# Optimization experiments

Measured on AMD Instinct MI355X. Metric: run time of the kernel, lower is better.

The kernel has to match this reference:

```python
import jax, jax.numpy as jnp
import numpy as np

B, L, N, C = 32, 12, 2048, 3
D = 64          # embed_dim
TOPK = 8
NK = 16         # n_kernel
TOD = 288
DOW = 7
OUT = 12        # output_len
NLAYER = 3
HS = 3 * D + TOPK * D + D        # spatial_hidden_dim = 768
HT = 4 * D + TOPK * D + D        # temporal_hidden_dim = 832
HC = int(100 * 0.1 * np.log(N / 0.1))  # EmbeddingTrainer bottleneck = 99
EPS = 1e-8


def setup_inputs() -> dict:
    key = jax.random.key(0)
    ks = jax.random.split(key, 20)
    r = lambda i, shape, s=0.02: jax.random.normal(ks[i], shape, jnp.float32) * s
    return dict(
        history_data=jax.random.uniform(ks[0], (B, L, N, C), jnp.float32),
        future_data=jax.random.uniform(ks[1], (B, OUT, N, C), jnp.float32),
        node_emb=r(2, (N, D), 0.1),
        et_w1=r(3, (HC, N)), et_b1=jnp.zeros((HC,), jnp.float32),
        et_w2=r(4, (N, HC)), et_b2=jnp.zeros((N,), jnp.float32),
        tod_emb=r(5, (TOD, D), 0.1), dow_emb=r(6, (DOW, D), 0.1),
        ts_w=r(7, (D, L), 0.1),
        feature_emb=r(8, (NK, D), 0.1),
        kernels=r(9, (NK, L), 0.1),
        sp_w=r(10, (D, HS)), sp_b=jnp.zeros((D,), jnp.float32),
        mlp_w1=r(11, (NLAYER, HT, HT), 0.01), mlp_b1=jnp.zeros((NLAYER, HT), jnp.float32),
        mlp_w2=r(12, (NLAYER, HT, HT), 0.01), mlp_b2=jnp.zeros((NLAYER, HT), jnp.float32),
        treg_w=r(13, (OUT, L), 0.1), treg_b=jnp.zeros((OUT,), jnp.float32),
        sreg_w=r(14, (OUT, HT), 0.02), sreg_b=jnp.zeros((OUT,), jnp.float32),
        daily_data=r(15, (TOD, N), 0.01), weekly_data=r(16, (DOW, N), 0.01),
        w_spatial=jnp.full((N,), 0.5, jnp.float32),
        batch_seen=0, epoch=0, train=1,
    )


def _forward(history_data, future_data, node_emb, et_w1, et_b1, et_w2, et_b2,
             tod_emb, dow_emb, ts_w, feature_emb, kernels, sp_w, sp_b,
             mlp_w1, mlp_b1, mlp_w2, mlp_b2, treg_w, treg_b, sreg_w, sreg_b,
             daily_data, weekly_data, w_spatial):
    x_in = history_data[..., 0]                              # (B,L,N)
    # --- temporal embeddings at last step ---
    tod_idx = (history_data[:, -1, :, 1] * TOD).astype(jnp.int32)   # (B,N)
    dow_idx = (history_data[:, -1, :, 2] * DOW).astype(jnp.int32)
    tid = tod_emb[tod_idx]                                   # (B,N,D)
    diw = dow_emb[dow_idx]
    # --- time-series embedding (1x1 conv over L channels) ---
    ts_emb = jnp.einsum('bln,dl->bdn', x_in, ts_w)           # (B,D,N)
    # --- EmbeddingTrainer: compress/reconstruct along node axis ---
    z = jax.nn.relu(jnp.einsum('nd,hn->dh', node_emb, et_w1) + et_b1)   # (D,HC)
    proj_node = (jnp.einsum('dh,nh->dn', z, et_w2) + et_b2).T           # (N,D)
    # --- NFConnection: cosine correlation node-series vs kernel bank ---
    xn = x_in / (jnp.linalg.norm(x_in, axis=1, keepdims=True) + EPS)
    kn = kernels / (jnp.linalg.norm(kernels, axis=1, keepdims=True) + EPS)
    conn = jnp.einsum('bln,kl->bnk', xn, kn)                 # (B,N,NK)
    c_weight, c_index = jax.lax.top_k(conn, TOPK)            # (B,N,TOPK)
    corr = jax.nn.sigmoid(c_weight)[..., None] * feature_emb[c_index]   # (B,N,TOPK,D)
    corr_ch = corr.reshape(B, N, TOPK * D).transpose(0, 2, 1)           # (B,TOPK*D,N)
    Hinc = jax.nn.one_hot(c_index, NK, dtype=jnp.float32).sum(axis=2)   # (B,N,NK)
    # --- assemble spatial encoder input ---
    node_ch = jnp.broadcast_to(proj_node.T[None], (B, D, N))
    enc_in = jnp.concatenate([ts_emb, node_ch, tid.transpose(0, 2, 1),
                              diw.transpose(0, 2, 1), corr_ch], axis=1)  # (B,HS,N)
    # --- SpatiaEncoder: 1x1 proj + hypergraph message passing ---
    h0 = jax.nn.relu(jnp.einsum('bcn,dc->bdn', enc_in, sp_w) + sp_b[None, :, None])
    deg_e = jnp.maximum(Hinc.sum(axis=1), 1.0)               # (B,NK)
    edge = jnp.einsum('bnk,bdn->bdk', Hinc, h0) / deg_e[:, None, :]
    edge = edge + feature_emb.T[None]                        # add hyperedge (kernel) embeddings
    msg = jnp.einsum('bnk,bdk->bdn', Hinc, edge) / TOPK
    sp_out = h0 + msg + proj_node.T[None]                    # (B,D,N)
    # --- temporal encoder: residual MLP stack ---
    h = jnp.concatenate([enc_in, sp_out], axis=1)            # (B,HT,N)
    for i in range(NLAYER):
        z1 = jax.nn.relu(jnp.einsum('bcn,dc->bdn', h, mlp_w1[i]) + mlp_b1[i][None, :, None])
        h = h + jnp.einsum('bcn,dc->bdn', z1, mlp_w2[i]) + mlp_b2[i][None, :, None]
    forecast_sp = jnp.einsum('bcn,oc->bon', h, sreg_w) + sreg_b[None, :, None]  # (B,OUT,N)
    # --- temporal branch: RevIN + daily/weekly cycle queues ---
    di_b = (history_data[:, :, 0, 1] * TOD).astype(jnp.int32)   # (B,L)
    wi_b = (history_data[:, :, 0, 2] * DOW).astype(jnp.int32)
    mean = x_in.mean(axis=1, keepdims=True)                  # (B,1,N)
    var = jnp.var(x_in, axis=1, keepdims=True, ddof=1) + 1e-5
    xr = (x_in - mean) / jnp.sqrt(var) - (daily_data[di_b] + weekly_data[wi_b])
    forecast_t = jnp.einsum('bln,ol->bon', xr, treg_w) + treg_b[None, :, None]
    di_f = (future_data[:, :, 0, 1] * TOD).astype(jnp.int32)
    wi_f = (future_data[:, :, 0, 2] * DOW).astype(jnp.int32)
    forecast_t = forecast_t + daily_data[di_f] + weekly_data[wi_f]
    forecast_t = forecast_t * jnp.sqrt(var) + mean
    pred = w_spatial[None, None, :] * forecast_sp + (1.0 - w_spatial)[None, None, :] * forecast_t
    return pred[..., None]                                   # (B,OUT,N,1)


def reference(history_data, future_data, node_emb, et_w1, et_b1, et_w2, et_b2,
              tod_emb, dow_emb, ts_w, feature_emb, kernels, sp_w, sp_b,
              mlp_w1, mlp_b1, mlp_w2, mlp_b2, treg_w, treg_b, sreg_w, sreg_b,
              daily_data, weekly_data, w_spatial, batch_seen, epoch, train):
    return _forward(history_data, future_data, node_emb, et_w1, et_b1, et_w2, et_b2,
                    tod_emb, dow_emb, ts_w, feature_emb, kernels, sp_w, sp_b,
                    mlp_w1, mlp_b1, mlp_w2, mlp_b2, treg_w, treg_b, sreg_w, sreg_b,
                    daily_data, weekly_data, w_spatial)
```

## Files before the change

### kernel.cpp

```cpp
#include <hip/hip_runtime.h>
#include <hip/hip_bf16.h>
#include <math.h>

#define BB 32
#define LL 12
#define NN 2048
#define DD 64
#define TOPK 8
#define NKER 16
#define OUTL 12
#define HS 768
#define HT 832
#define HTP 896
#define HCB 99
#define BN (BB*NN)

typedef __attribute__((ext_vector_type(8))) short bf16x8;
typedef __attribute__((ext_vector_type(4))) float f32x4;

#define GLOAD16(gp, lp) __builtin_amdgcn_global_load_lds( \
    (const __attribute__((address_space(1))) unsigned int*)(uintptr_t)(gp), \
    (__attribute__((address_space(3))) unsigned int*)(unsigned int)(uintptr_t)(lp), \
    16, 0, 0)

__global__ __launch_bounds__(256)
void f2b_pad_kernel(const float* __restrict__ x, __hip_bfloat16* __restrict__ y,
                    int rows, int cols, int prows) {
    int i = blockIdx.x * 256 + threadIdx.x;
    if (i >= prows * cols) return;
    int r = i / cols;
    y[i] = __float2bfloat16((r < rows) ? x[i] : 0.f);
}

__global__ __launch_bounds__(64)
void et_z_kernel(const float* __restrict__ node_emb, const float* __restrict__ w1,
                 const float* __restrict__ b1, float* __restrict__ z) {
    int hh = blockIdx.x;
    int d  = threadIdx.x;
    float acc = 0.f;
    for (int nn = 0; nn < NN; ++nn)
        acc += node_emb[nn*DD + d] * w1[(size_t)hh*NN + nn];
    acc += b1[hh];
    z[d*HCB + hh] = fmaxf(acc, 0.f);
}

__global__ __launch_bounds__(64)
void et_proj_kernel(const float* __restrict__ z, const float* __restrict__ w2,
                    const float* __restrict__ b2, float* __restrict__ proj) {
    int nn = blockIdx.x;
    int d  = threadIdx.x;
    float acc = 0.f;
    for (int hh = 0; hh < HCB; ++hh)
        acc += z[d*HCB + hh] * w2[nn*HCB + hh];
    proj[nn*DD + d] = acc + b2[nn];
}

__global__ __launch_bounds__(64)
void prep_kernel(const float* __restrict__ hist, const float* __restrict__ proj,
                 const float* __restrict__ tod_emb, const float* __restrict__ dow_emb,
                 const float* __restrict__ ts_w, const float* __restrict__ feat_emb,
                 const float* __restrict__ kern, __hip_bfloat16* __restrict__ h,
                 int* __restrict__ cidx, unsigned int* __restrict__ mask) {
    const int tok = blockIdx.x;
    const int b = tok >> 11, n = tok & (NN-1);
    const int lane = threadIdx.x;
    __shared__ float xs[LL];
    __shared__ float conn_s[NKER];
    __shared__ int   idx_s[TOPK];
    __shared__ float w_s[TOPK];

    if (lane < LL)
        xs[lane] = hist[((size_t)(b*LL + lane) * NN + n) * 3];
    __syncthreads();

    if (lane < NKER) {
        float xn = 0.f;
        #pragma unroll
        for (int l = 0; l < LL; ++l) xn += xs[l]*xs[l];
        xn = sqrtf(xn) + 1e-8f;
        float kn = 0.f;
        #pragma unroll
        for (int l = 0; l < LL; ++l) { float kv = kern[lane*LL + l]; kn += kv*kv; }
        kn = sqrtf(kn) + 1e-8f;
        float dot = 0.f;
        #pragma unroll
        for (int l = 0; l < LL; ++l) dot += (xs[l]/xn) * (kern[lane*LL + l]/kn);
        conn_s[lane] = dot;
    }
    __syncthreads();

    if (lane == 0) {
        float c[NKER];
        #pragma unroll
        for (int k = 0; k < NKER; ++k) c[k] = conn_s[k];
        unsigned int mk = 0;
        for (int j = 0; j < TOPK; ++j) {
            float best = -1e30f; int bi = 0;
            #pragma unroll
            for (int k = 0; k < NKER; ++k)
                if (c[k] > best) { best = c[k]; bi = k; }
            idx_s[j] = bi;
            w_s[j] = 1.f / (1.f + expf(-best));
            c[bi] = -1e30f;
            mk |= (1u << bi);
            cidx[(size_t)tok*TOPK + j] = bi;
        }
        mask[tok] = mk;
    }
    __syncthreads();

    const int d = lane;
    float ts = 0.f;
    #pragma unroll
    for (int l = 0; l < LL; ++l) ts += xs[l] * ts_w[d*LL + l];
    size_t base = (size_t)tok * HT;
    h[base + d] = __float2bfloat16(ts);
    h[base + DD + d] = __float2bfloat16(proj[n*DD + d]);
    size_t last = ((size_t)(b*LL + (LL-1)) * NN + n) * 3;
    int ti = (int)(hist[last + 1] * 288.f);
    int wi = (int)(hist[last + 2] * 7.f);
    h[base + 2*DD + d] = __float2bfloat16(tod_emb[ti*DD + d]);
    h[base + 3*DD + d] = __float2bfloat16(dow_emb[wi*DD + d]);
    #pragma unroll
    for (int j = 0; j < TOPK; ++j)
        h[base + 4*DD + j*DD + d] = __float2bfloat16(w_s[j] * feat_emb[idx_s[j]*DD + d]);
}

template<int RELU, int ACCUM, int CF32, int NCOLS, int NJ>
__global__ __launch_bounds__(256, 4)
void gemm128(const unsigned short* __restrict__ A, int lda,
             const unsigned short* __restrict__ W, int ldb,
             const float* __restrict__ bias,
             void* __restrict__ Cp, int ldc, int K, int ntiles) {
    __shared__ __align__(16) unsigned short As[128*64];
    __shared__ __align__(16) unsigned short Bs[128*64];

    int nwg = gridDim.x, bid = blockIdx.x;
    int q = nwg >> 3, r = nwg & 7;
    int xcd = bid & 7, idx = bid >> 3;
    int swz = ((xcd < r) ? xcd*(q+1) : r*(q+1) + (xcd-r)*q) + idx;
    const long long m0 = (long long)(swz / ntiles) * 128;
    const int n0 = (swz % ntiles) * (NJ*32);

    const int tid = threadIdx.x;
    const int wave = tid >> 6, lane = tid & 63;
    const int wr = wave >> 1, wc = wave & 1;
    const int l15 = lane & 15, l4 = lane >> 4;

    const int srow = tid >> 3;
    const int gc = ((tid & 7) ^ ((tid >> 3) & 7)) * 8;
    const unsigned short* ag = A + (m0 + srow) * (long long)lda + gc;
    const unsigned short* bg = W + (long long)(n0 + srow) * ldb + gc;

    f32x4 acc[4][NJ] = {};

    for (int k0 = 0; k0 < K; k0 += 64) {
        #pragma unroll
        for (int qq = 0; qq < 4; ++qq)
            GLOAD16(ag + k0 + (long long)(qq*32)*lda, &As[(qq*256 + tid)*8]);
        #pragma unroll
        for (int qq = 0; qq < NJ; ++qq)
            GLOAD16(bg + k0 + (long long)(qq*32)*ldb, &Bs[(qq*256 + tid)*8]);
        __syncthreads();
        #pragma unroll
        for (int kh = 0; kh < 2; ++kh) {
            bf16x8 af[4], bf[NJ];
            #pragma unroll
            for (int i = 0; i < 4; ++i) {
                int ra = wr*64 + i*16 + l15;
                af[i] = *(const bf16x8*)&As[ra*64 + (((kh*4 + l4) ^ (ra & 7)) * 8)];
            }
            #pragma unroll
            for (int j = 0; j < NJ; ++j) {
                int rb = wc*(NJ*16) + j*16 + l15;
                bf[j] = *(const bf16x8*)&Bs[rb*64 + (((kh*4 + l4) ^ (rb & 7)) * 8)];
            }
            #pragma unroll
            for (int i = 0; i < 4; ++i)
                #pragma unroll
                for (int j = 0; j < NJ; ++j)
                    acc[i][j] = __builtin_amdgcn_mfma_f32_16x16x32_bf16(af[i], bf[j], acc[i][j], 0, 0, 0);
        }
        __syncthreads();
    }

    float* Cf = (float*)Cp;
    __hip_bfloat16* Cb = (__hip_bfloat16*)Cp;
    #pragma unroll
    for (int i = 0; i < 4; ++i) {
        #pragma unroll
        for (int j = 0; j < NJ; ++j) {
            int col = n0 + wc*(NJ*16) + j*16 + l15;
            if (col < NCOLS) {
                float bv = bias[col];
                #pragma unroll
                for (int rg = 0; rg < 4; ++rg) {
                    long long row = m0 + wr*64 + i*16 + l4*4 + rg;
                    float v = acc[i][j][rg] + bv;
                    if (RELU) v = fmaxf(v, 0.f);
                    if (CF32) {
                        Cf[row*ldc + col] = v;
                    } else {
                        if (ACCUM) v += __bfloat162float(Cb[row*ldc + col]);
                        Cb[row*ldc + col] = __float2bfloat16(v);
                    }
                }
            }
        }
    }
}

__global__ __launch_bounds__(256)
void edge_kernel(const float* __restrict__ h0, const unsigned int* __restrict__ mask,
                 const float* __restrict__ feat_emb, float* __restrict__ edge) {
    int b = blockIdx.x >> 4, k = blockIdx.x & 15;
    int g = threadIdx.x >> 6, d = threadIdx.x & 63;
    __shared__ float accs[4][64];
    __shared__ int cnts[4];
    float acc = 0.f; int cnt = 0;
    size_t tb = (size_t)b * NN;
    #pragma unroll 4
    for (int nn = g; nn < NN; nn += 4) {
        unsigned int bit = (mask[tb + nn] >> k) & 1u;
        acc += (float)bit * h0[(tb + nn)*DD + d];
        cnt += (int)bit;
    }
    accs[g][d] = acc;
    if (d == 0) cnts[g] = cnt;
    __syncthreads();
    if (g == 0) {
        float a = accs[0][d] + accs[1][d] + accs[2][d] + accs[3][d];
        int c = cnts[0] + cnts[1] + cnts[2] + cnts[3];
        edge[((size_t)b*NKER + k)*DD + d] = a / fmaxf((float)c, 1.f) + feat_emb[k*DD + d];
    }
}

__global__ __launch_bounds__(256)
void msg_kernel(const float* __restrict__ h0, const float* __restrict__ edge,
                const int* __restrict__ cidx, const float* __restrict__ proj,
                __hip_bfloat16* __restrict__ h) {
    __shared__ float eS[NKER*DD];
    int t0 = blockIdx.x * 4;
    int b = t0 >> 11;
    for (int i = threadIdx.x; i < NKER*DD; i += 256) eS[i] = edge[(size_t)b*NKER*DD + i];
    __syncthreads();
    int g = threadIdx.x >> 6, lane = threadIdx.x & 63;
    int tok = t0 + g, n = tok & (NN-1);
    float m = 0.f;
    #pragma unroll
    for (int j = 0; j < TOPK; ++j)
        m += eS[cidx[(size_t)tok*TOPK + j]*DD + lane];
    float sp = h0[(size_t)tok*DD + lane] + m*0.125f + proj[n*DD + lane];
    h[(size_t)tok*HT + HS + lane] = __float2bfloat16(sp);
}

__global__ __launch_bounds__(256)
void temporal_kernel(const float* __restrict__ hist, const float* __restrict__ fut,
                     const float* __restrict__ daily, const float* __restrict__ weekly,
                     const float* __restrict__ treg_w, const float* __restrict__ treg_b,
                     float* __restrict__ outp) {
    __shared__ int s_di[LL], s_wi[LL], s_df[OUTL], s_wf[OUTL];
    __shared__ float s_tw[OUTL*LL], s_tb[OUTL];
    int tid = threadIdx.x;
    int tok = blockIdx.x * 256 + tid;
    int b = tok >> 11, n = tok & (NN-1);
    if (tid < LL) {
        size_t hb = ((size_t)(b*LL + tid) * NN) * 3;
        s_di[tid] = (int)(hist[hb + 1] * 288.f);
        s_wi[tid] = (int)(hist[hb + 2] * 7.f);
        size_t fb = ((size_t)(b*OUTL + tid) * NN) * 3;
        s_df[tid] = (int)(fut[fb + 1] * 288.f);
        s_wf[tid] = (int)(fut[fb + 2] * 7.f);
        s_tb[tid] = treg_b[tid];
    }
    if (tid < OUTL*LL) s_tw[tid] = treg_w[tid];
    __syncthreads();
    float x[LL];
    float mean = 0.f;
    #pragma unroll
    for (int l = 0; l < LL; ++l) {
        x[l] = hist[((size_t)(b*LL + l) * NN + n) * 3];
        mean += x[l];
    }
    mean *= (1.f/12.f);
    float ss = 0.f;
    #pragma unroll
    for (int l = 0; l < LL; ++l) { float dd = x[l]-mean; ss += dd*dd; }
    float sd = sqrtf(ss*(1.f/11.f) + 1e-5f);
    float xr[LL];
    #pragma unroll
    for (int l = 0; l < LL; ++l)
        xr[l] = (x[l]-mean)/sd - daily[(size_t)s_di[l]*NN + n] - weekly[(size_t)s_wi[l]*NN + n];
    #pragma unroll
    for (int o = 0; o < OUTL; ++o) {
        float f = s_tb[o];
        #pragma unroll
        for (int l = 0; l < LL; ++l) f += xr[l]*s_tw[o*LL + l];
        f += daily[(size_t)s_df[o]*NN + n] + weekly[(size_t)s_wf[o]*NN + n];
        f = f*sd + mean;
        outp[((size_t)b*OUTL + o)*NN + n] = f;
    }
}

__global__ __launch_bounds__(256)
void final_kernel(const __hip_bfloat16* __restrict__ h, const float* __restrict__ sreg_w,
                  const float* __restrict__ sreg_b, const float* __restrict__ w_sp,
                  float* __restrict__ outp) {
    int g = threadIdx.x >> 6, lane = threadIdx.x & 63;
    int tok = blockIdx.x*4 + g;
    int b = tok >> 11, n = tok & (NN-1);
    float acc[OUTL];
    #pragma unroll
    for (int o = 0; o < OUTL; ++o) acc[o] = 0.f;
    size_t base = (size_t)tok * HT;
    for (int c = lane; c < HT; c += 64) {
        float hv = __bfloat162float(h[base + c]);
        #pragma unroll
        for (int o = 0; o < OUTL; ++o) acc[o] += hv * sreg_w[o*HT + c];
    }
    #pragma unroll
    for (int o = 0; o < OUTL; ++o) {
        #pragma unroll
        for (int s = 32; s >= 1; s >>= 1)
            acc[o] += __shfl_xor(acc[o], s, 64);
    }
    float v = 0.f;
    #pragma unroll
    for (int o = 0; o < OUTL; ++o) if (lane == o) v = acc[o] + sreg_b[o];
    if (lane < OUTL) {
        size_t oi = ((size_t)b*OUTL + lane)*NN + n;
        float t = outp[oi];
        float w = w_sp[n];
        outp[oi] = w*v + (1.f-w)*t;
    }
}

extern "C" void kernel_launch(void* const* d_in, const int* in_sizes, int n_in,
                              void* d_out, int out_size, void* d_ws, size_t ws_size,
                              hipStream_t stream) {
    const float* hist    = (const float*)d_in[0];
    const float* fut     = (const float*)d_in[1];
    const float* node_emb= (const float*)d_in[2];
    const float* et_w1   = (const float*)d_in[3];
    const float* et_b1   = (const float*)d_in[4];
    const float* et_w2   = (const float*)d_in[5];
    const float* et_b2   = (const float*)d_in[6];
    const float* tod_emb = (const float*)d_in[7];
    const float* dow_emb = (const float*)d_in[8];
    const float* ts_w    = (const float*)d_in[9];
    const float* feat    = (const float*)d_in[10];
    const float* kern    = (const float*)d_in[11];
    const float* sp_w    = (const float*)d_in[12];
    const float* sp_b    = (const float*)d_in[13];
    const float* mlp_w1  = (const float*)d_in[14];
    const float* mlp_b1  = (const float*)d_in[15];
    const float* mlp_w2  = (const float*)d_in[16];
    const float* mlp_b2  = (const float*)d_in[17];
    const float* treg_w  = (const float*)d_in[18];
    const float* treg_b  = (const float*)d_in[19];
    const float* sreg_w  = (const float*)d_in[20];
    const float* sreg_b  = (const float*)d_in[21];
    const float* daily   = (const float*)d_in[22];
    const float* weekly  = (const float*)d_in[23];
    const float* w_sp    = (const float*)d_in[24];
    float* out = (float*)d_out;

    char* ws = (char*)d_ws;
    __hip_bfloat16* h    = (__hip_bfloat16*)(ws);
    float*          h0   = (float*)(ws + 109051904ULL);
    float*          proj = (float*)(ws + 125829120ULL);
    float*          zet  = (float*)(ws + 126353408ULL);
    float*          edge = (float*)(ws + 126386176ULL);
    int*            cidx = (int*)  (ws + 126517248ULL);
    unsigned int*   mask = (unsigned int*)(ws + 128614400ULL);
    __hip_bfloat16* spwb = (__hip_bfloat16*)(ws + 128876544ULL);
    __hip_bfloat16* w1b  = (__hip_bfloat16*)(ws + 129073152ULL);
    __hip_bfloat16* w2b  = (__hip_bfloat16*)(ws + 133545984ULL);
    const size_t z1_off = 138018816ULL;
    __hip_bfloat16* z1   = (__hip_bfloat16*)(ws + z1_off);

    long long avail = (ws_size > z1_off) ? (long long)(ws_size - z1_off) : 0;
    long long chunk = (avail / (HT*2)) & ~127LL;
    if (chunk > BN) chunk = BN;
    if (chunk < 128) chunk = 128;

    f2b_pad_kernel<<<(128*HS + 255)/256, 256, 0, stream>>>(sp_w, spwb, 64, HS, 128);
    for (int i = 0; i < 3; ++i) {
        f2b_pad_kernel<<<(HTP*HT + 255)/256, 256, 0, stream>>>(
            mlp_w1 + (size_t)i*HT*HT, w1b + (size_t)i*HTP*HT, HT, HT, HTP);
        f2b_pad_kernel<<<(HTP*HT + 255)/256, 256, 0, stream>>>(
            mlp_w2 + (size_t)i*HT*HT, w2b + (size_t)i*HTP*HT, HT, HT, HTP);
    }

    et_z_kernel  <<<HCB, 64, 0, stream>>>(node_emb, et_w1, et_b1, zet);
    et_proj_kernel<<<NN, 64, 0, stream>>>(zet, et_w2, et_b2, proj);
    prep_kernel  <<<BN, 64, 0, stream>>>(hist, proj, tod_emb, dow_emb, ts_w, feat, kern,
                                         h, cidx, mask);
    gemm128<1,0,1,64,2><<<BN/128, 256, 0, stream>>>(
        (const unsigned short*)h, HT, (const unsigned short*)spwb, HS, sp_b, h0, DD, HS, 1);
    edge_kernel  <<<BB*NKER, 256, 0, stream>>>(h0, mask, feat, edge);
    msg_kernel   <<<BN/4, 256, 0, stream>>>(h0, edge, cidx, proj, h);
    for (int i = 0; i < 3; ++i) {
        for (long long ms = 0; ms < BN; ms += chunk) {
            long long mm = (BN - ms < chunk) ? (BN - ms) : chunk;
            int grid = (int)(mm/128) * (HTP/128);
            gemm128<1,0,0,HT,4><<<grid, 256, 0, stream>>>(
                (const unsigned short*)(h + ms*HT), HT,
                (const unsigned short*)(w1b + (size_t)i*HTP*HT), HT,
                mlp_b1 + i*HT, z1, HT, HT, HTP/128);
            gemm128<0,1,0,HT,4><<<grid, 256, 0, stream>>>(
                (const unsigned short*)z1, HT,
                (const unsigned short*)(w2b + (size_t)i*HTP*HT), HT,
                mlp_b2 + i*HT, h + ms*HT, HT, HT, HTP/128);
        }
    }
    temporal_kernel<<<BN/256, 256, 0, stream>>>(hist, fut, daily, weekly, treg_w, treg_b, out);
    final_kernel <<<BN/4, 256, 0, stream>>>(h, sreg_w, sreg_b, w_sp, out);
}
```

Baseline: 1.079 ms.

## Switch GEMMs to 32x32x16 MFMA and drop padded N tile for MLP

The GEMM kernel now uses 32x32x16 bf16 MFMA instructions with larger per-wave fragments instead of 16x16x32, which cuts LDS fragment reads per FLOP. The MLP weight padding from 832 to 896 rows is removed. Each MLP GEMM is split into a 768-column launch with 128-wide N tiles plus a 64-column tail launch, so the padded columns are no longer computed. The cost is two extra launches per layer and a small tail grid that may underfill the device.

```diff
diff --git a/kernel.cpp b/kernel.cpp
--- a/kernel.cpp
+++ b/kernel.cpp
@@ -11,12 +11,11 @@
 #define OUTL 12
 #define HS 768
 #define HT 832
-#define HTP 896
 #define HCB 99
 #define BN (BB*NN)
 
 typedef __attribute__((ext_vector_type(8))) short bf16x8;
-typedef __attribute__((ext_vector_type(4))) float f32x4;
+typedef __attribute__((ext_vector_type(16))) float f32x16;
 
 #define GLOAD16(gp, lp) __builtin_amdgcn_global_load_lds( \
     (const __attribute__((address_space(1))) unsigned int*)(uintptr_t)(gp), \
@@ -24,12 +23,9 @@
     16, 0, 0)
 
 __global__ __launch_bounds__(256)
-void f2b_pad_kernel(const float* __restrict__ x, __hip_bfloat16* __restrict__ y,
-                    int rows, int cols, int prows) {
+void f2b_kernel(const float* __restrict__ x, __hip_bfloat16* __restrict__ y, int n) {
     int i = blockIdx.x * 256 + threadIdx.x;
-    if (i >= prows * cols) return;
-    int r = i / cols;
-    y[i] = __float2bfloat16((r < rows) ? x[i] : 0.f);
+    if (i < n) y[i] = __float2bfloat16(x[i]);
 }
 
 __global__ __launch_bounds__(64)
@@ -126,12 +122,12 @@
         h[base + 4*DD + j*DD + d] = __float2bfloat16(w_s[j] * feat_emb[idx_s[j]*DD + d]);
 }
 
-template<int RELU, int ACCUM, int CF32, int NCOLS, int NJ>
+template<int RELU, int ACCUM, int CF32, int NJF>
 __global__ __launch_bounds__(256, 4)
-void gemm128(const unsigned short* __restrict__ A, int lda,
-             const unsigned short* __restrict__ W, int ldb,
-             const float* __restrict__ bias,
-             void* __restrict__ Cp, int ldc, int K, int ntiles) {
+void gemm_m32(const unsigned short* __restrict__ A, int lda,
+              const unsigned short* __restrict__ W, int ldb,
+              const float* __restrict__ bias,
+              void* __restrict__ Cp, int ldc, int K, int ntiles) {
     __shared__ __align__(16) unsigned short As[128*64];
     __shared__ __align__(16) unsigned short Bs[128*64];
 
@@ -140,46 +136,46 @@
     int xcd = bid & 7, idx = bid >> 3;
     int swz = ((xcd < r) ? xcd*(q+1) : r*(q+1) + (xcd-r)*q) + idx;
     const long long m0 = (long long)(swz / ntiles) * 128;
-    const int n0 = (swz % ntiles) * (NJ*32);
+    const int n0 = (swz % ntiles) * (NJF*64);
 
     const int tid = threadIdx.x;
     const int wave = tid >> 6, lane = tid & 63;
     const int wr = wave >> 1, wc = wave & 1;
-    const int l15 = lane & 15, l4 = lane >> 4;
+    const int l31 = lane & 31, l32 = lane >> 5;
 
     const int srow = tid >> 3;
     const int gc = ((tid & 7) ^ ((tid >> 3) & 7)) * 8;
     const unsigned short* ag = A + (m0 + srow) * (long long)lda + gc;
     const unsigned short* bg = W + (long long)(n0 + srow) * ldb + gc;
 
-    f32x4 acc[4][NJ] = {};
+    f32x16 acc[2][NJF] = {};
 
     for (int k0 = 0; k0 < K; k0 += 64) {
         #pragma unroll
         for (int qq = 0; qq < 4; ++qq)
             GLOAD16(ag + k0 + (long long)(qq*32)*lda, &As[(qq*256 + tid)*8]);
         #pragma unroll
-        for (int qq = 0; qq < NJ; ++qq)
+        for (int qq = 0; qq < NJF*2; ++qq)
             GLOAD16(bg + k0 + (long long)(qq*32)*ldb, &Bs[(qq*256 + tid)*8]);
         __syncthreads();
         #pragma unroll
-        for (int kh = 0; kh < 2; ++kh) {
-            bf16x8 af[4], bf[NJ];
+        for (int ks = 0; ks < 4; ++ks) {
+            bf16x8 af[2], bf[NJF];
             #pragma unroll
-            for (int i = 0; i < 4; ++i) {
-                int ra = wr*64 + i*16 + l15;
-                af[i] = *(const bf16x8*)&As[ra*64 + (((kh*4 + l4) ^ (ra & 7)) * 8)];
+            for (int i = 0; i < 2; ++i) {
+                int ra = wr*64 + i*32 + l31;
+                af[i] = *(const bf16x8*)&As[ra*64 + (((ks*2 + l32) ^ (ra & 7)) * 8)];
             }
             #pragma unroll
-            for (int j = 0; j < NJ; ++j) {
-                int rb = wc*(NJ*16) + j*16 + l15;
-                bf[j] = *(const bf16x8*)&Bs[rb*64 + (((kh*4 + l4) ^ (rb & 7)) * 8)];
+            for (int j = 0; j < NJF; ++j) {
+                int rb = wc*(NJF*32) + j*32 + l31;
+                bf[j] = *(const bf16x8*)&Bs[rb*64 + (((ks*2 + l32) ^ (rb & 7)) * 8)];
             }
             #pragma unroll
-            for (int i = 0; i < 4; ++i)
+            for (int i = 0; i < 2; ++i)
                 #pragma unroll
-                for (int j = 0; j < NJ; ++j)
-                    acc[i][j] = __builtin_amdgcn_mfma_f32_16x16x32_bf16(af[i], bf[j], acc[i][j], 0, 0, 0);
+                for (int j = 0; j < NJF; ++j)
+                    acc[i][j] = __builtin_amdgcn_mfma_f32_32x32x16_bf16(af[i], bf[j], acc[i][j], 0, 0, 0);
         }
         __syncthreads();
     }
@@ -187,23 +183,21 @@
     float* Cf = (float*)Cp;
     __hip_bfloat16* Cb = (__hip_bfloat16*)Cp;
     #pragma unroll
-    for (int i = 0; i < 4; ++i) {
-        #pragma unroll
-        for (int j = 0; j < NJ; ++j) {
-            int col = n0 + wc*(NJ*16) + j*16 + l15;
-            if (col < NCOLS) {
-                float bv = bias[col];
-                #pragma unroll
-                for (int rg = 0; rg < 4; ++rg) {
-                    long long row = m0 + wr*64 + i*16 + l4*4 + rg;
-                    float v = acc[i][j][rg] + bv;
-                    if (RELU) v = fmaxf(v, 0.f);
-                    if (CF32) {
-                        Cf[row*ldc + col] = v;
-                    } else {
-                        if (ACCUM) v += __bfloat162float(Cb[row*ldc + col]);
-                        Cb[row*ldc + col] = __float2bfloat16(v);
-                    }
+    for (int i = 0; i < 2; ++i) {
+        #pragma unroll
+        for (int j = 0; j < NJF; ++j) {
+            int col = n0 + wc*(NJF*32) + j*32 + l31;
+            float bv = bias[col];
+            #pragma unroll
+            for (int rg = 0; rg < 16; ++rg) {
+                long long row = m0 + wr*64 + i*32 + (rg & 3) + 8*(rg >> 2) + 4*l32;
+                float v = acc[i][j][rg] + bv;
+                if (RELU) v = fmaxf(v, 0.f);
+                if (CF32) {
+                    Cf[row*ldc + col] = v;
+                } else {
+                    if (ACCUM) v += __bfloat162float(Cb[row*ldc + col]);
+                    Cb[row*ldc + col] = __float2bfloat16(v);
                 }
             }
         }
@@ -384,34 +378,35 @@
     if (chunk > BN) chunk = BN;
     if (chunk < 128) chunk = 128;
 
-    f2b_pad_kernel<<<(128*HS + 255)/256, 256, 0, stream>>>(sp_w, spwb, 64, HS, 128);
-    for (int i = 0; i < 3; ++i) {
-        f2b_pad_kernel<<<(HTP*HT + 255)/256, 256, 0, stream>>>(
-            mlp_w1 + (size_t)i*HT*HT, w1b + (size_t)i*HTP*HT, HT, HT, HTP);
-        f2b_pad_kernel<<<(HTP*HT + 255)/256, 256, 0, stream>>>(
-            mlp_w2 + (size_t)i*HT*HT, w2b + (size_t)i*HTP*HT, HT, HT, HTP);
-    }
+    f2b_kernel<<<(64*HS + 255)/256, 256, 0, stream>>>(sp_w, spwb, 64*HS);
+    f2b_kernel<<<(3*HT*HT + 255)/256, 256, 0, stream>>>(mlp_w1, w1b, 3*HT*HT);
+    f2b_kernel<<<(3*HT*HT + 255)/256, 256, 0, stream>>>(mlp_w2, w2b, 3*HT*HT);
 
     et_z_kernel  <<<HCB, 64, 0, stream>>>(node_emb, et_w1, et_b1, zet);
     et_proj_kernel<<<NN, 64, 0, stream>>>(zet, et_w2, et_b2, proj);
     prep_kernel  <<<BN, 64, 0, stream>>>(hist, proj, tod_emb, dow_emb, ts_w, feat, kern,
                                          h, cidx, mask);
-    gemm128<1,0,1,64,2><<<BN/128, 256, 0, stream>>>(
+    gemm_m32<1,0,1,1><<<BN/128, 256, 0, stream>>>(
         (const unsigned short*)h, HT, (const unsigned short*)spwb, HS, sp_b, h0, DD, HS, 1);
     edge_kernel  <<<BB*NKER, 256, 0, stream>>>(h0, mask, feat, edge);
     msg_kernel   <<<BN/4, 256, 0, stream>>>(h0, edge, cidx, proj, h);
     for (int i = 0; i < 3; ++i) {
+        const unsigned short* W1 = (const unsigned short*)(w1b + (size_t)i*HT*HT);
+        const unsigned short* W2 = (const unsigned short*)(w2b + (size_t)i*HT*HT);
         for (long long ms = 0; ms < BN; ms += chunk) {
             long long mm = (BN - ms < chunk) ? (BN - ms) : chunk;
-            int grid = (int)(mm/128) * (HTP/128);
-            gemm128<1,0,0,HT,4><<<grid, 256, 0, stream>>>(
-                (const unsigned short*)(h + ms*HT), HT,
-                (const unsigned short*)(w1b + (size_t)i*HTP*HT), HT,
-                mlp_b1 + i*HT, z1, HT, HT, HTP/128);
-            gemm128<0,1,0,HT,4><<<grid, 256, 0, stream>>>(
-                (const unsigned short*)z1, HT,
-                (const unsigned short*)(w2b + (size_t)i*HTP*HT), HT,
-                mlp_b2 + i*HT, h + ms*HT, HT, HT, HTP/128);
+            int mb = (int)(mm/128);
+            const unsigned short* Ah = (const unsigned short*)(h + ms*HT);
+            gemm_m32<1,0,0,2><<<mb*6, 256, 0, stream>>>(
+                Ah, HT, W1, HT, mlp_b1 + i*HT, z1, HT, HT, 6);
+            gemm_m32<1,0,0,1><<<mb, 256, 0, stream>>>(
+                Ah, HT, W1 + (size_t)768*HT, HT, mlp_b1 + i*HT + 768, z1 + 768, HT, HT, 1);
+            gemm_m32<0,1,0,2><<<mb*6, 256, 0, stream>>>(
+                (const unsigned short*)z1, HT, W2, HT, mlp_b2 + i*HT,
+                (void*)(h + ms*HT), HT, HT, 6);
+            gemm_m32<0,1,0,1><<<mb, 256, 0, stream>>>(
+                (const unsigned short*)z1, HT, W2 + (size_t)768*HT, HT, mlp_b2 + i*HT + 768,
+                (void*)(h + ms*HT + 768), HT, HT, 1);
         }
     }
     temporal_kernel<<<BN/256, 256, 0, stream>>>(hist, fut, daily, weekly, treg_w, treg_b, out);
```

Result: slower. 1.173 ms (+8.7%).
